# Kernel tuning notes

Measured on AMD Instinct MI355X. Metric: run time of the kernel, lower is better.

Reference implementation:

```python
import jax, jax.numpy as jnp
import numpy as np

R = 2            # interleaving factor (init kwarg r)
C = 16           # feature channels
N = 500_000      # number of sparse voxels
GRID = 256       # fine-grid extent per axis


def setup_inputs() -> dict:
    key = jax.random.key(0)
    kc, kf = jax.random.split(key)
    coords = jax.random.randint(kc, (N, 3), 0, GRID, dtype=jnp.int32)
    feats = jax.random.normal(kf, (N, C), dtype=jnp.float32)
    return {"feats": feats, "coords": coords}


def reference(feats, coords):
    # Sparse interleaving: group fine voxels into coarse voxels of size R^3,
    # scattering each point's C features into the slot given by its intra-cell offset.
    r2 = R * R
    r3 = r2 * R
    n = coords.shape[0]
    base = coords // R                      # [N,3] coarse voxel coords
    off = coords % R                        # [N,3] intra-cell offset
    offset_idx = off[:, 0] * r2 + off[:, 1] * R + off[:, 2]  # [N]

    # jit-compatible unique: fixed output size (worst case: all points distinct)
    unique_coords, inv = jnp.unique(base, axis=0, size=n, fill_value=-1,
                                    return_inverse=True)
    inv = inv.reshape(-1)                   # [N] row in aggregated output

    # target column = offset_idx*C + channel  (matches torch scatter_ layout)
    col = offset_idx[:, None] * C + jnp.arange(C, dtype=offset_idx.dtype)[None, :]  # [N,C]
    agg = jnp.zeros((n, C * r3), dtype=feats.dtype)
    agg = agg.at[inv[:, None], col].set(feats)
    return unique_coords.astype(jnp.int32), agg
```

## Files before the change

### kernel.cpp

```cpp
#include <hip/hip_runtime.h>


#define WORDS 65536u

__global__ void mark_kernel(const int* __restrict__ coords,
                            unsigned* __restrict__ bitmap, int n) {
    int i = blockIdx.x * 256 + threadIdx.x;
    if (i >= n) return;
    int cx = coords[3 * i], cy = coords[3 * i + 1], cz = coords[3 * i + 2];
    unsigned key = ((unsigned)(cx >> 1) << 14) | ((unsigned)(cy >> 1) << 7) |
                   (unsigned)(cz >> 1);
    atomicOr(&bitmap[key >> 5], 1u << (key & 31));
}

__global__ void chunksum_kernel(const unsigned* __restrict__ bitmap,
                                unsigned* __restrict__ chunkSum) {
    __shared__ unsigned sh[256];
    int t = threadIdx.x;
    sh[t] = __popc(bitmap[blockIdx.x * 256 + t]);
    __syncthreads();
    for (int d = 128; d > 0; d >>= 1) {
        if (t < d) sh[t] += sh[t + d];
        __syncthreads();
    }
    if (t == 0) chunkSum[blockIdx.x] = sh[0];
}

__global__ void scan_kernel(unsigned* chunkSum, unsigned* U) {
    __shared__ unsigned sh[256];
    int t = threadIdx.x;
    unsigned s = chunkSum[t];
    unsigned x = s;
    sh[t] = x; __syncthreads();
    for (int d = 1; d < 256; d <<= 1) {
        unsigned y = (t >= d) ? sh[t - d] : 0u;
        __syncthreads();
        x += y; sh[t] = x; __syncthreads();
    }
    chunkSum[t] = x - s;
    if (t == 255) *U = x;
}

__global__ void rank_coords_kernel(const unsigned* __restrict__ bitmap,
                                   const unsigned* __restrict__ chunkExcl,
                                   unsigned* __restrict__ rank_base,
                                   float* __restrict__ coords_out) {
    __shared__ unsigned sh[256];
    int t = threadIdx.x;
    unsigned w = blockIdx.x * 256 + t;
    unsigned word = bitmap[w];
    unsigned cnt = __popc(word);
    unsigned x = cnt;
    sh[t] = x; __syncthreads();
    for (int d = 1; d < 256; d <<= 1) {
        unsigned y = (t >= d) ? sh[t - d] : 0u;
        __syncthreads();
        x += y; sh[t] = x; __syncthreads();
    }
    unsigned rb = chunkExcl[blockIdx.x] + x - cnt;
    rank_base[w] = rb;
    while (word) {
        int k = __ffs(word) - 1;
        word &= word - 1;
        unsigned cell = w * 32u + (unsigned)k;
        coords_out[3 * rb + 0] = (float)(cell >> 14);
        coords_out[3 * rb + 1] = (float)((cell >> 7) & 127u);
        coords_out[3 * rb + 2] = (float)(cell & 127u);
        ++rb;
    }
}

__global__ void pad_kernel(const unsigned* __restrict__ U,
                           float* __restrict__ coords_out, int n) {
    int i = blockIdx.x * 256 + threadIdx.x;
    if (i < n && (unsigned)i >= *U) {
        coords_out[3 * i + 0] = -1.0f;
        coords_out[3 * i + 1] = -1.0f;
        coords_out[3 * i + 2] = -1.0f;
    }
}

__global__ void winner_kernel(const int* __restrict__ coords,
                              const unsigned* __restrict__ bitmap,
                              const unsigned* __restrict__ rank_base,
                              int* __restrict__ winner, int n) {
    int i = blockIdx.x * 256 + threadIdx.x;
    if (i >= n) return;
    int cx = coords[3 * i], cy = coords[3 * i + 1], cz = coords[3 * i + 2];
    unsigned key = ((unsigned)(cx >> 1) << 14) | ((unsigned)(cy >> 1) << 7) |
                   (unsigned)(cz >> 1);
    unsigned off = ((unsigned)(cx & 1) << 2) | ((unsigned)(cy & 1) << 1) |
                   (unsigned)(cz & 1);
    unsigned wd = key >> 5;
    unsigned r = rank_base[wd] + __popc(bitmap[wd] & ((1u << (key & 31)) - 1u));
    atomicMax(&winner[r * 8u + off], i);
}

__global__ void gather_kernel(const float* __restrict__ feats,
                              const int* __restrict__ winner,
                              float* __restrict__ agg, int total4) {
    int j = blockIdx.x * 256 + threadIdx.x;
    if (j >= total4) return;
    int slot = j >> 2;
    int c4 = j & 3;
    int w = winner[slot];
    float4 v = make_float4(0.f, 0.f, 0.f, 0.f);
    if (w >= 0) v = ((const float4*)feats)[(size_t)w * 4 + c4];
    ((float4*)agg)[j] = v;
}

extern "C" void kernel_launch(void* const* d_in, const int* in_sizes, int n_in,
                              void* d_out, int out_size, void* d_ws, size_t ws_size,
                              hipStream_t stream) {
    const float* feats = (const float*)d_in[0];
    const int* coords  = (const int*)d_in[1];
    int n = in_sizes[1] / 3;

    float* out        = (float*)d_out;
    float* coords_out = out;
    float* agg        = out + (size_t)3 * n;

    unsigned* bitmap    = (unsigned*)d_ws;
    unsigned* rank_base = bitmap + WORDS;
    unsigned* chunkSum  = rank_base + WORDS;
    unsigned* U         = chunkSum + 256;
    int*      winner    = (int*)(U + 4);

    hipMemsetAsync(bitmap, 0, WORDS * sizeof(unsigned), stream);
    hipMemsetAsync(winner, 0xFF, (size_t)8 * n * sizeof(int), stream);

    int nb = (n + 255) / 256;
    mark_kernel<<<nb, 256, 0, stream>>>(coords, bitmap, n);
    chunksum_kernel<<<WORDS / 256, 256, 0, stream>>>(bitmap, chunkSum);
    scan_kernel<<<1, 256, 0, stream>>>(chunkSum, U);
    rank_coords_kernel<<<WORDS / 256, 256, 0, stream>>>(bitmap, chunkSum,
                                                        rank_base, coords_out);
    pad_kernel<<<nb, 256, 0, stream>>>(U, coords_out, n);
    winner_kernel<<<nb, 256, 0, stream>>>(coords, bitmap, rank_base, winner, n);
    int total4 = n * 32;
    gather_kernel<<<(total4 + 255) / 256, 256, 0, stream>>>(feats, winner, agg,
                                                            total4);
}
```

Baseline: 376.2 us.

## Fuse winner init, chunk scan and padding kernels; use nontemporal gather stores

Folds the winner-array memset into the mark kernel with a grid-stride loop, merges the chunk popcount and scan into a single-block kernel, and merges the coordinate padding into the rank kernel. The gather kernel now uses nontemporal loads and stores for the winner index and the large aggregated output. The aim is to cut launch count and the separate memset pass. The trade-off is that the single-block scan now reads the whole bitmap serially (each thread does 256 popcounts), which could take longer than the old multi-block chunk sum.

```diff
diff --git a/kernel.cpp b/kernel.cpp
--- a/kernel.cpp
+++ b/kernel.cpp
@@ -3,9 +3,14 @@
 
 #define WORDS 65536u
 
-__global__ void mark_kernel(const int* __restrict__ coords,
-                            unsigned* __restrict__ bitmap, int n) {
+typedef float v4f __attribute__((ext_vector_type(4)));
+
+__global__ void mark_init_kernel(const int* __restrict__ coords,
+                                 unsigned* __restrict__ bitmap,
+                                 int* __restrict__ winner, int n) {
     int i = blockIdx.x * 256 + threadIdx.x;
+    int nthreads = gridDim.x * 256;
+    for (int s = i; s < 8 * n; s += nthreads) winner[s] = -1;
     if (i >= n) return;
     int cx = coords[3 * i], cy = coords[3 * i + 1], cz = coords[3 * i + 2];
     unsigned key = ((unsigned)(cx >> 1) << 14) | ((unsigned)(cy >> 1) << 7) |
@@ -13,23 +18,15 @@
     atomicOr(&bitmap[key >> 5], 1u << (key & 31));
 }
 
-__global__ void chunksum_kernel(const unsigned* __restrict__ bitmap,
-                                unsigned* __restrict__ chunkSum) {
+__global__ void scanall_kernel(const unsigned* __restrict__ bitmap,
+                               unsigned* __restrict__ chunkExcl,
+                               unsigned* __restrict__ U) {
     __shared__ unsigned sh[256];
     int t = threadIdx.x;
-    sh[t] = __popc(bitmap[blockIdx.x * 256 + t]);
-    __syncthreads();
-    for (int d = 128; d > 0; d >>= 1) {
-        if (t < d) sh[t] += sh[t + d];
-        __syncthreads();
-    }
-    if (t == 0) chunkSum[blockIdx.x] = sh[0];
-}
-
-__global__ void scan_kernel(unsigned* chunkSum, unsigned* U) {
-    __shared__ unsigned sh[256];
-    int t = threadIdx.x;
-    unsigned s = chunkSum[t];
+    unsigned s = 0;
+    unsigned base = (unsigned)t * 256u;
+#pragma unroll 8
+    for (unsigned j = 0; j < 256u; ++j) s += __popc(bitmap[base + j]);
     unsigned x = s;
     sh[t] = x; __syncthreads();
     for (int d = 1; d < 256; d <<= 1) {
@@ -37,14 +34,15 @@
         __syncthreads();
         x += y; sh[t] = x; __syncthreads();
     }
-    chunkSum[t] = x - s;
+    chunkExcl[t] = x - s;
     if (t == 255) *U = x;
 }
 
-__global__ void rank_coords_kernel(const unsigned* __restrict__ bitmap,
-                                   const unsigned* __restrict__ chunkExcl,
-                                   unsigned* __restrict__ rank_base,
-                                   float* __restrict__ coords_out) {
+__global__ void rank_coords_pad_kernel(const unsigned* __restrict__ bitmap,
+                                       const unsigned* __restrict__ chunkExcl,
+                                       const unsigned* __restrict__ U,
+                                       unsigned* __restrict__ rank_base,
+                                       float* __restrict__ coords_out, int n) {
     __shared__ unsigned sh[256];
     int t = threadIdx.x;
     unsigned w = blockIdx.x * 256 + t;
@@ -68,12 +66,9 @@
         coords_out[3 * rb + 2] = (float)(cell & 127u);
         ++rb;
     }
-}
-
-__global__ void pad_kernel(const unsigned* __restrict__ U,
-                           float* __restrict__ coords_out, int n) {
-    int i = blockIdx.x * 256 + threadIdx.x;
-    if (i < n && (unsigned)i >= *U) {
+    unsigned u = *U;
+    int nthreads = gridDim.x * 256;
+    for (unsigned i = u + w; i < (unsigned)n; i += nthreads) {
         coords_out[3 * i + 0] = -1.0f;
         coords_out[3 * i + 1] = -1.0f;
         coords_out[3 * i + 2] = -1.0f;
@@ -103,10 +98,10 @@
     if (j >= total4) return;
     int slot = j >> 2;
     int c4 = j & 3;
-    int w = winner[slot];
-    float4 v = make_float4(0.f, 0.f, 0.f, 0.f);
-    if (w >= 0) v = ((const float4*)feats)[(size_t)w * 4 + c4];
-    ((float4*)agg)[j] = v;
+    int w = __builtin_nontemporal_load(&winner[slot]);
+    v4f v = (v4f)(0.f);
+    if (w >= 0) v = ((const v4f*)feats)[(size_t)w * 4 + c4];
+    __builtin_nontemporal_store(v, (v4f*)agg + j);
 }
 
 extern "C" void kernel_launch(void* const* d_in, const int* in_sizes, int n_in,
@@ -122,20 +117,17 @@
 
     unsigned* bitmap    = (unsigned*)d_ws;
     unsigned* rank_base = bitmap + WORDS;
-    unsigned* chunkSum  = rank_base + WORDS;
-    unsigned* U         = chunkSum + 256;
+    unsigned* chunkExcl = rank_base + WORDS;
+    unsigned* U         = chunkExcl + 256;
     int*      winner    = (int*)(U + 4);
 
-    hipMemsetAsync(bitmap, 0, WORDS * sizeof(unsigned), stream);
-    hipMemsetAsync(winner, 0xFF, (size_t)8 * n * sizeof(int), stream);
+    (void)hipMemsetAsync(bitmap, 0, WORDS * sizeof(unsigned), stream);
 
     int nb = (n + 255) / 256;
-    mark_kernel<<<nb, 256, 0, stream>>>(coords, bitmap, n);
-    chunksum_kernel<<<WORDS / 256, 256, 0, stream>>>(bitmap, chunkSum);
-    scan_kernel<<<1, 256, 0, stream>>>(chunkSum, U);
-    rank_coords_kernel<<<WORDS / 256, 256, 0, stream>>>(bitmap, chunkSum,
-                                                        rank_base, coords_out);
-    pad_kernel<<<nb, 256, 0, stream>>>(U, coords_out, n);
+    mark_init_kernel<<<nb, 256, 0, stream>>>(coords, bitmap, winner, n);
+    scanall_kernel<<<1, 256, 0, stream>>>(bitmap, chunkExcl, U);
+    rank_coords_pad_kernel<<<WORDS / 256, 256, 0, stream>>>(bitmap, chunkExcl, U,
+                                                            rank_base, coords_out, n);
     winner_kernel<<<nb, 256, 0, stream>>>(coords, bitmap, rank_base, winner, n);
     int total4 = n * 32;
     gather_kernel<<<(total4 + 255) / 256, 256, 0, stream>>>(feats, winner, agg,
```

After: 372.2 us. No clear change (-1.1%).
